# Kernel tuning notes

Measured on AMD Instinct MI355X. Metric: run time of the kernel, lower is better.

The kernel has to match this reference:

```python
import jax, jax.numpy as jnp
import numpy as np

N_NODES = 100_000
N_HYPEREDGES = 200_000
NNZ = 2_000_000
D = 64
H = 32
KEEP_RATIO = 0.5


def setup_inputs() -> dict:
    key = jax.random.key(0)
    ks = jax.random.split(key, 5)
    x = jax.random.normal(ks[0], (N_NODES, D), jnp.float32)
    V_idx = jax.random.randint(ks[1], (NNZ,), 0, N_NODES)
    E_idx = jax.random.randint(ks[2], (NNZ,), 0, N_HYPEREDGES)
    W1 = jax.random.normal(ks[3], (2 * D, H), jnp.float32) * (1.0 / np.sqrt(2 * D))
    b1 = jnp.zeros((H,), jnp.float32)
    W2 = jax.random.normal(ks[4], (H, 1), jnp.float32) * (1.0 / np.sqrt(H))
    b2 = jnp.zeros((1,), jnp.float32)
    return dict(x=x, V_idx=V_idx, E_idx=E_idx, W1=W1, b1=b1, W2=W2, b2=b2)


def _segment_mean(vals, idx, num_segments):
    # index_add sum / clamped count, matching reduce_incidence_to_edge / index_mean
    s = jax.ops.segment_sum(vals, idx, num_segments=num_segments)
    c = jax.ops.segment_sum(jnp.ones((vals.shape[0],), vals.dtype), idx,
                            num_segments=num_segments)
    c = jnp.clip(c, 1.0, None)
    if vals.ndim == 2:
        c = c[:, None]
    return s / c


def reference(x, V_idx, E_idx, W1, b1, W2, b2):
    xv = x[V_idx]                                   # [nnz, D] gather
    edge_feats = _segment_mean(xv, E_idx, N_HYPEREDGES)  # [E, D]
    pair = jnp.concatenate([xv, edge_feats[E_idx]], axis=-1)  # [nnz, 2D]
    h = jax.nn.relu(pair @ W1 + b1)                 # [nnz, H]
    probs = jax.nn.sigmoid((h @ W2 + b2)[:, 0])     # [nnz]

    k = max(1, int(KEEP_RATIO * NNZ))
    keep_ids = jax.lax.top_k(probs, k)[1]           # is_test=True path (deterministic)
    hard = jnp.zeros_like(probs).at[keep_ids].set(1.0)
    soft = jax.lax.stop_gradient(hard - probs) + probs  # straight-through

    edge_probs = _segment_mean(jax.lax.stop_gradient(probs), E_idx, N_HYPEREDGES)
    edge_soft = _segment_mean(soft, E_idx, N_HYPEREDGES)
    edge_hard = (_segment_mean(hard, E_idx, N_HYPEREDGES) > 0).astype(jnp.float32)
    return (probs, soft, hard, edge_probs, edge_soft, edge_hard)
```

## Files before the change

kernel.cpp:

```cpp
#include <hip/hip_runtime.h>
#include <math.h>

#define N_NODES   100000
#define N_EDGES   200000
#define NNZ       2000000
#define K_KEEP    1000000
#define BANDCAP   131072
#define TIECAP    4096
#define DELTA     1.0e-4f
#define SCAN_BLOCKS 196
#define USCALE (4294967296.0 / 4.0e-3)

#define SC_PASSES 8
#define SC_EPP    (N_EDGES / SC_PASSES)
#define SC_BLOCKS 2048

#define OFF_PAB   ((size_t)0)
#define OFF_PB32  ((size_t)25600000)
#define OFF_VJ    ((size_t)33600000)
#define OFF_RANK  ((size_t)49600000)
#define OFF_EOFF  ((size_t)57600000)
#define OFF_CUR   ((size_t)58400000)
#define OFF_BS    ((size_t)59200000)
#define OFF_BANDP ((size_t)59201024)
#define OFF_BANDJ ((size_t)59725312)
#define OFF_BANDE ((size_t)60249600)
#define OFF_BANDV ((size_t)60773888)
#define OFF_BANDK ((size_t)61298176)
#define OFF_TIEK  ((size_t)62346752)
#define OFF_TIEJ  ((size_t)62379520)
#define OFF_TIEP  ((size_t)62395904)
#define OFF_FLAG  ((size_t)62412288)
#define OFF_ECNT  ((size_t)64412288)
#define OFF_HIST  ((size_t)65212288)
#define OFF_ST    ((size_t)65245056)
#define ZERO_OFF  OFF_FLAG
#define ZERO_LEN  ((size_t)(65245312 - 62412288))

struct SelState {
    unsigned int B1;
    unsigned int rem1;
    float lo_edge, hi_edge;
    unsigned int bB1;
    unsigned int brem1;
    unsigned int bU0;
    unsigned int brem2;
    unsigned int _pad0[8];
    unsigned int n_hi;      unsigned int _pad1[15];
    unsigned int band_n;    unsigned int _pad2[15];
    unsigned int tie_n;     unsigned int _pad3[15];
};

__device__ __forceinline__ unsigned int band_u32(double key, float lo) {
    double t = (key - (double)lo) * USCALE;
    t = t < 0.0 ? 0.0 : (t > 4294967295.0 ? 4294967295.0 : t);
    return (unsigned int)t;
}

__global__ void proj_kernel(const float* __restrict__ x, const float* __restrict__ W1,
                            float2* __restrict__ p_ab2) {
    __shared__ float sW[128 * 32];
    __shared__ float sx[8][64];
    for (int t = threadIdx.x; t < 128 * 32; t += 256) sW[t] = W1[t];
    int base = blockIdx.x * 8;
    for (int t = threadIdx.x; t < 512; t += 256) {
        int n = t >> 6, d = t & 63;
        int g = base + n;
        sx[n][d] = (g < N_NODES) ? x[(size_t)g * 64 + d] : 0.f;
    }
    __syncthreads();
    int ln = threadIdx.x >> 5;
    int k  = threadIdx.x & 31;
    int node = base + ln;
    if (node >= N_NODES) return;
    float sa = 0.f, sb = 0.f;
    for (int d = 0; d < 64; ++d) {
        float xv = sx[ln][d];
        sa += xv * sW[d * 32 + k];
        sb += xv * sW[(64 + d) * 32 + k];
    }
    p_ab2[(size_t)node * 32 + k] = make_float2(sa, sb);
}

__global__ void count_rank_kernel(const int* __restrict__ E, unsigned int* __restrict__ edge_cnt,
                                  unsigned int* __restrict__ rank) {
    unsigned int base = blockIdx.x * 2048 + threadIdx.x;
    int ev[8];
    unsigned int rr[8];
    #pragma unroll
    for (int c = 0; c < 8; ++c) {
        unsigned int j = base + 256u * c;
        if (j < NNZ) ev[c] = E[j];
    }
    #pragma unroll
    for (int c = 0; c < 8; ++c) {
        unsigned int j = base + 256u * c;
        if (j < NNZ) rr[c] = atomicAdd(&edge_cnt[ev[c]], 1u);
    }
    #pragma unroll
    for (int c = 0; c < 8; ++c) {
        unsigned int j = base + 256u * c;
        if (j < NNZ) rank[j] = rr[c];
    }
}

__global__ void scanA_kernel(const unsigned int* __restrict__ edge_cnt,
                             unsigned int* __restrict__ edge_off, unsigned int* __restrict__ bsums) {
    __shared__ unsigned int s[256];
    int tid = threadIdx.x;
    int base = blockIdx.x * 1024 + tid * 4;
    unsigned int v0 = (base + 0 < N_EDGES) ? edge_cnt[base + 0] : 0u;
    unsigned int v1 = (base + 1 < N_EDGES) ? edge_cnt[base + 1] : 0u;
    unsigned int v2 = (base + 2 < N_EDGES) ? edge_cnt[base + 2] : 0u;
    unsigned int v3 = (base + 3 < N_EDGES) ? edge_cnt[base + 3] : 0u;
    unsigned int tsum = v0 + v1 + v2 + v3;
    s[tid] = tsum;
    __syncthreads();
    for (int off = 1; off < 256; off <<= 1) {
        unsigned int t = (tid >= off) ? s[tid - off] : 0u;
        __syncthreads();
        s[tid] += t;
        __syncthreads();
    }
    unsigned int excl = s[tid] - tsum;
    if (base + 0 < N_EDGES) edge_off[base + 0] = excl;
    if (base + 1 < N_EDGES) edge_off[base + 1] = excl + v0;
    if (base + 2 < N_EDGES) edge_off[base + 2] = excl + v0 + v1;
    if (base + 3 < N_EDGES) edge_off[base + 3] = excl + v0 + v1 + v2;
    if (tid == 255) bsums[blockIdx.x] = s[255];
}

__global__ void scanB_kernel(unsigned int* __restrict__ bsums) {
    __shared__ unsigned int s[256];
    int tid = threadIdx.x;
    unsigned int v = (tid < SCAN_BLOCKS) ? bsums[tid] : 0u;
    s[tid] = v;
    __syncthreads();
    for (int off = 1; off < 256; off <<= 1) {
        unsigned int t = (tid >= off) ? s[tid - off] : 0u;
        __syncthreads();
        s[tid] += t;
        __syncthreads();
    }
    if (tid < SCAN_BLOCKS) bsums[tid] = s[tid] - v;
}

__global__ void scanC_kernel(unsigned int* __restrict__ edge_off, const unsigned int* __restrict__ bsums) {
    int i = blockIdx.x * 256 + threadIdx.x;
    if (i >= N_EDGES) return;
    edge_off[i] = edge_off[i] + bsums[i >> 10];
}

__global__ void scatter_kernel(const int* __restrict__ V, const int* __restrict__ E,
                               const unsigned int* __restrict__ edge_off,
                               const unsigned int* __restrict__ rank,
                               uint2* __restrict__ vj) {
    unsigned int pass = blockIdx.x & 7u;
    unsigned int q    = blockIdx.x >> 3;
    unsigned int elo  = pass * SC_EPP;
    const unsigned int stride = (SC_BLOCKS / 8) * 256;
    for (unsigned int j = q * 256u + threadIdx.x; j < NNZ; j += stride) {
        unsigned int e = (unsigned int)__builtin_nontemporal_load(E + j);
        if (e - elo < (unsigned int)SC_EPP) {
            unsigned int pp = edge_off[e] + __builtin_nontemporal_load(rank + j);
            unsigned int v  = (unsigned int)__builtin_nontemporal_load(V + j);
            vj[pp] = make_uint2(v, j);
        }
    }
}

__global__ void edge_logit_kernel(const uint2* __restrict__ vj,
                                  const unsigned int* __restrict__ edge_off,
                                  const unsigned int* __restrict__ edge_cnt,
                                  const float2* __restrict__ p_ab2,
                                  const float* __restrict__ b1, const float* __restrict__ W2,
                                  const float* __restrict__ b2,
                                  float* __restrict__ probs_b, float* __restrict__ o_ep) {
    __shared__ float slog[4][32];
    __shared__ unsigned int sv[4][32];
    int e = blockIdx.x * 4 + (threadIdx.x >> 6);
    if (e >= N_EDGES) return;
    int w    = threadIdx.x >> 6;
    int lane = threadIdx.x & 63;
    int g    = lane >> 4;
    int l    = lane & 15;

    unsigned int off = edge_off[e];
    unsigned int deg = edge_cnt[e];
    unsigned int mind = deg < 32u ? deg : 32u;

    if ((unsigned int)lane < mind) sv[w][lane] = vj[off + lane].x;

    float2 w2  = ((const float2*)W2)[l];
    float2 bb1 = ((const float2*)b1)[l];
    float  b2v = b2[0];

    float2 aA[8];
    float2 bacc = make_float2(0.f, 0.f);
    #pragma unroll 8
    for (unsigned int m = 0; m < 8u; ++m) {
        if (4u * m >= mind) break;
        unsigned int idx = 4u * m + (unsigned int)g;
        if (idx < mind) {
            unsigned int v = sv[w][idx];
            float4 r = reinterpret_cast<const float4*>(p_ab2 + (size_t)v * 32u)[l];
            aA[m] = make_float2(r.x, r.z);
            bacc.x += r.y;
            bacc.y += r.w;
        } else {
            aA[m] = make_float2(0.f, 0.f);
        }
    }
    for (unsigned int ii = 32u + (unsigned int)g; ii < deg; ii += 4u) {
        unsigned int v = vj[off + ii].x;
        float4 r = reinterpret_cast<const float4*>(p_ab2 + (size_t)v * 32u)[l];
        bacc.x += r.y;
        bacc.y += r.w;
    }
    bacc.x += __shfl_xor(bacc.x, 16);
    bacc.y += __shfl_xor(bacc.y, 16);
    bacc.x += __shfl_xor(bacc.x, 32);
    bacc.y += __shfl_xor(bacc.y, 32);
    float cc = (float)(deg > 1u ? deg : 1u);
    float2 em2 = make_float2(bacc.x / cc + bb1.x, bacc.y / cc + bb1.y);

    #pragma unroll 8
    for (unsigned int m = 0; m < 8u; ++m) {
        if (4u * m >= mind) break;
        unsigned int idx = 4u * m + (unsigned int)g;
        float h0 = aA[m].x + em2.x;
        float h1 = aA[m].y + em2.y;
        h0 = h0 > 0.f ? h0 : 0.f;
        h1 = h1 > 0.f ? h1 : 0.f;
        float t = h0 * w2.x + h1 * w2.y;
        #pragma unroll
        for (int o = 8; o > 0; o >>= 1) t += __shfl_down(t, o, 16);
        if (l == 0 && idx < mind) slog[w][idx] = t;
    }
    float prsum = 0.f;
    if ((unsigned int)lane < mind) {
        float pr = 1.f / (1.f + __expf(-(slog[w][lane] + b2v)));
        probs_b[off + lane] = pr;
        prsum = pr;
    }
    for (unsigned int ii = 32u + (unsigned int)g; ii < deg; ii += 4u) {
        unsigned int v = vj[off + ii].x;
        float4 r = reinterpret_cast<const float4*>(p_ab2 + (size_t)v * 32u)[l];
        float h0 = r.x + em2.x;
        float h1 = r.z + em2.y;
        h0 = h0 > 0.f ? h0 : 0.f;
        h1 = h1 > 0.f ? h1 : 0.f;
        float t = h0 * w2.x + h1 * w2.y;
        #pragma unroll
        for (int o = 8; o > 0; o >>= 1) t += __shfl_down(t, o, 16);
        if (l == 0) {
            float pr = 1.f / (1.f + __expf(-(t + b2v)));
            probs_b[off + ii] = pr;
            prsum += pr;
        }
    }
    #pragma unroll
    for (int o = 32; o > 0; o >>= 1) prsum += __shfl_down(prsum, o, 64);
    if (lane == 0) o_ep[e] = prsum / cc;
}

__global__ void hist1_kernel(const float* __restrict__ probs_b, unsigned int* __restrict__ hist) {
    __shared__ unsigned int lh[2048];
    for (int t = threadIdx.x; t < 2048; t += 256) lh[t] = 0;
    __syncthreads();
    for (unsigned int i = blockIdx.x * 256 + threadIdx.x; i < NNZ; i += gridDim.x * 256) {
        unsigned int key = __float_as_uint(probs_b[i]);
        atomicAdd(&lh[key >> 21], 1u);
    }
    __syncthreads();
    for (int t = threadIdx.x; t < 2048; t += 256)
        if (lh[t]) atomicAdd(&hist[t], lh[t]);
}

__global__ void hist2_kernel(const float* __restrict__ probs_b, const SelState* __restrict__ st,
                             unsigned int* __restrict__ hist) {
    __shared__ unsigned int lh[2048];
    for (int t = threadIdx.x; t < 2048; t += 256) lh[t] = 0;
    __syncthreads();
    unsigned int B1 = st->B1;
    for (unsigned int i = blockIdx.x * 256 + threadIdx.x; i < NNZ; i += gridDim.x * 256) {
        unsigned int key = __float_as_uint(probs_b[i]);
        if ((key >> 21) == B1) atomicAdd(&lh[(key >> 10) & 2047u], 1u);
    }
    __syncthreads();
    for (int t = threadIdx.x; t < 2048; t += 256)
        if (lh[t]) atomicAdd(&hist[2048 + t], lh[t]);
}

__global__ void scan_sel_kernel(const unsigned int* __restrict__ hist, SelState* __restrict__ st, int which) {
    __shared__ unsigned int csum[256];
    int t = threadIdx.x;
    unsigned int target = (which == 0) ? (unsigned int)K_KEEP : st->rem1;
    const unsigned int* h = hist + (which ? 2048 : 0);
    unsigned int b[8];
    unsigned int s = 0;
    #pragma unroll
    for (int i = 0; i < 8; ++i) { b[i] = h[t * 8 + i]; s += b[i]; }
    csum[t] = s;
    __syncthreads();
    for (int off = 1; off < 256; off <<= 1) {
        unsigned int v = (t + off < 256) ? csum[t + off] : 0u;
        __syncthreads();
        csum[t] += v;
        __syncthreads();
    }
    unsigned int above = csum[t] - s;
    if (above < target && target <= above + s) {
        unsigned int rem = target - above;
        unsigned int cum = 0;
        #pragma unroll
        for (int i = 7; i >= 0; --i) {
            if (rem <= cum + b[i]) {
                unsigned int bin = (unsigned int)(t * 8 + i);
                if (which == 0) { st->B1 = bin; st->rem1 = rem - cum; }
                else {
                    unsigned int P = (st->B1 << 21) | (bin << 10);
                    st->lo_edge = __uint_as_float(P) - DELTA;
                    st->hi_edge = __uint_as_float(P + 1024u) + DELTA;
                }
                break;
            }
            cum += b[i];
        }
    }
}

__global__ void bandsel_kernel(const float* __restrict__ probs_b, const int* __restrict__ E,
                               const uint2* __restrict__ vj,
                               SelState* __restrict__ st,
                               unsigned int* __restrict__ band_p, unsigned int* __restrict__ band_j,
                               unsigned int* __restrict__ band_e, unsigned int* __restrict__ band_v) {
    __shared__ unsigned int whi[4], wband[4];
    __shared__ unsigned int sbase, scur;
    float hi = st->hi_edge, lo = st->lo_edge;
    unsigned int nhi = 0, nband = 0;
    for (unsigned int p = blockIdx.x * 256 + threadIdx.x; p < NNZ; p += gridDim.x * 256) {
        float pk = probs_b[p];
        if (pk > hi) nhi++;
        else if (pk >= lo) nband++;
    }
    #pragma unroll
    for (int o = 32; o > 0; o >>= 1) {
        nhi   += __shfl_down(nhi, o);
        nband += __shfl_down(nband, o);
    }
    if ((threadIdx.x & 63) == 0) { whi[threadIdx.x >> 6] = nhi; wband[threadIdx.x >> 6] = nband; }
    __syncthreads();
    if (threadIdx.x == 0) {
        unsigned int th = whi[0] + whi[1] + whi[2] + whi[3];
        unsigned int tb = wband[0] + wband[1] + wband[2] + wband[3];
        if (th) atomicAdd(&st->n_hi, th);
        sbase = tb ? atomicAdd(&st->band_n, tb) : 0u;
        scur = 0;
    }
    __syncthreads();
    for (unsigned int p = blockIdx.x * 256 + threadIdx.x; p < NNZ; p += gridDim.x * 256) {
        float pk = probs_b[p];
        if (pk <= hi && pk >= lo) {
            unsigned int s = sbase + atomicAdd(&scur, 1u);
            if (s < BANDCAP) {
                uint2 t = vj[p];
                band_p[s] = p;
                band_j[s] = t.y;
                band_e[s] = (unsigned int)E[t.y];
                band_v[s] = t.x;
            }
        }
    }
}

__global__ void rescue_kernel(const uint2* __restrict__ vj,
                              const unsigned int* __restrict__ edge_off,
                              const unsigned int* __restrict__ edge_cnt,
                              const float* __restrict__ x, const float* __restrict__ W1,
                              const float* __restrict__ b1, const float* __restrict__ W2,
                              const float* __restrict__ b2,
                              const unsigned int* __restrict__ band_e,
                              const unsigned int* __restrict__ band_v,
                              const SelState* __restrict__ st,
                              unsigned long long* __restrict__ band_key) {
    unsigned int n = st->band_n; if (n > BANDCAP) n = BANDCAP;
    if (blockIdx.x * 8 >= n) return;
    __shared__ float sW[128 * 32];
    for (int t = threadIdx.x; t < 128 * 32; t += 256) sW[t] = W1[t];
    __syncthreads();
    unsigned int g = blockIdx.x * 8 + (threadIdx.x >> 5);
    if (g >= n) return;
    int k = threadIdx.x & 31;
    unsigned int v = band_v[g];
    unsigned int e = band_e[g];
    unsigned int off = edge_off[e];
    unsigned int deg = edge_cnt[e];

    const float* xv = x + (size_t)v * 64u;
    double a = 0.0;
    #pragma unroll 8
    for (int d = 0; d < 64; ++d) a += (double)xv[d] * (double)sW[d * 32 + k];
    double bsum = 0.0;
    for (unsigned int m = off; m < off + deg; ++m) {
        const float* xm = x + (size_t)vj[m].x * 64u;
        double acc = 0.0;
        #pragma unroll 8
        for (int d = 0; d < 64; ++d) acc += (double)xm[d] * (double)sW[(64 + d) * 32 + k];
        bsum += acc;
    }
    double cc = (double)(deg > 1u ? deg : 1u);
    double h = a + bsum / cc + (double)b1[k];
    h = h > 0.0 ? h : 0.0;
    double t = h * (double)W2[k];
    #pragma unroll
    for (int o = 16; o > 0; o >>= 1) t += __shfl_down(t, o, 32);
    if (k == 0) {
        double pr = 1.0 / (1.0 + exp(-(t + (double)b2[0])));
        band_key[g] = (unsigned long long)__double_as_longlong(pr);
    }
}

__global__ void bhist1_kernel(const unsigned long long* __restrict__ band_key,
                              const SelState* __restrict__ st, unsigned int* __restrict__ hist) {
    __shared__ unsigned int lh[2048];
    for (int t = threadIdx.x; t < 2048; t += 256) lh[t] = 0;
    __syncthreads();
    unsigned int n = st->band_n; if (n > BANDCAP) n = BANDCAP;
    float lo = st->lo_edge;
    for (unsigned int i = blockIdx.x * 256 + threadIdx.x; i < n; i += gridDim.x * 256) {
        unsigned int u = band_u32(__longlong_as_double((long long)band_key[i]), lo);
        atomicAdd(&lh[u >> 21], 1u);
    }
    __syncthreads();
    for (int t = threadIdx.x; t < 2048; t += 256)
        if (lh[t]) atomicAdd(&hist[4096 + t], lh[t]);
}

__global__ void bhist2_kernel(const unsigned long long* __restrict__ band_key,
                              const SelState* __restrict__ st, unsigned int* __restrict__ hist) {
    __shared__ unsigned int lh[2048];
    for (int t = threadIdx.x; t < 2048; t += 256) lh[t] = 0;
    __syncthreads();
    unsigned int n = st->band_n; if (n > BANDCAP) n = BANDCAP;
    float lo = st->lo_edge;
    unsigned int bB1 = st->bB1;
    for (unsigned int i = blockIdx.x * 256 + threadIdx.x; i < n; i += gridDim.x * 256) {
        unsigned int u = band_u32(__longlong_as_double((long long)band_key[i]), lo);
        if ((u >> 21) == bB1) atomicAdd(&lh[(u >> 10) & 2047u], 1u);
    }
    __syncthreads();
    for (int t = threadIdx.x; t < 2048; t += 256)
        if (lh[t]) atomicAdd(&hist[6144 + t], lh[t]);
}

__global__ void bscan_kernel(const unsigned int* __restrict__ hist, SelState* __restrict__ st, int which) {
    __shared__ unsigned int csum[256];
    int t = threadIdx.x;
    unsigned int target = (which == 0) ? ((unsigned int)K_KEEP - st->n_hi) : st->brem1;
    const unsigned int* h = hist + (which ? 6144 : 4096);
    unsigned int b[8];
    unsigned int s = 0;
    #pragma unroll
    for (int i = 0; i < 8; ++i) { b[i] = h[t * 8 + i]; s += b[i]; }
    csum[t] = s;
    __syncthreads();
    for (int off = 1; off < 256; off <<= 1) {
        unsigned int v = (t + off < 256) ? csum[t + off] : 0u;
        __syncthreads();
        csum[t] += v;
        __syncthreads();
    }
    unsigned int above = csum[t] - s;
    if (above < target && target <= above + s) {
        unsigned int rem = target - above;
        unsigned int cum = 0;
        #pragma unroll
        for (int i = 7; i >= 0; --i) {
            if (rem <= cum + b[i]) {
                unsigned int bin = (unsigned int)(t * 8 + i);
                if (which == 0) { st->bB1 = bin; st->brem1 = rem - cum; }
                else            { st->bU0 = (st->bB1 << 21) | (bin << 10); st->brem2 = rem - cum; }
                break;
            }
            cum += b[i];
        }
    }
}

__global__ void btie_kernel(const unsigned long long* __restrict__ band_key,
                            const unsigned int* __restrict__ band_j,
                            const unsigned int* __restrict__ band_p,
                            SelState* __restrict__ st, unsigned char* __restrict__ flag,
                            unsigned long long* __restrict__ tie_k,
                            unsigned int* __restrict__ tie_j, unsigned int* __restrict__ tie_p) {
    unsigned int n = st->band_n; if (n > BANDCAP) n = BANDCAP;
    unsigned int i = blockIdx.x * 256 + threadIdx.x;
    if (i >= n) return;
    float lo = st->lo_edge;
    unsigned int U0 = st->bU0;
    unsigned long long key = band_key[i];
    unsigned int u = band_u32(__longlong_as_double((long long)key), lo);
    if (u >= U0 + 1024u) {
        flag[band_p[i]] = 2u;
    } else if (u >= U0) {
        unsigned int s = atomicAdd(&st->tie_n, 1u);
        if (s < TIECAP) { tie_k[s] = key; tie_j[s] = band_j[i]; tie_p[s] = band_p[i]; }
    }
}

__global__ void btierank_kernel(const unsigned long long* __restrict__ tie_k,
                                const unsigned int* __restrict__ tie_j,
                                const unsigned int* __restrict__ tie_p,
                                const SelState* __restrict__ st, unsigned char* __restrict__ flag) {
    unsigned int n = st->tie_n; if (n > TIECAP) n = TIECAP;
    unsigned int need = st->brem2;
    for (unsigned int i = threadIdx.x; i < n; i += 256) {
        unsigned long long ki = tie_k[i];
        unsigned int ji = tie_j[i];
        unsigned int r = 0;
        for (unsigned int q = 0; q < n; ++q) {
            unsigned long long kq = tie_k[q];
            if (kq > ki || (kq == ki && tie_j[q] < ji)) r++;
        }
        if (r < need) flag[tie_p[i]] = 2u;
    }
}

__global__ void out_kernel(const float* __restrict__ probs_b, const unsigned char* __restrict__ flag,
                           const int* __restrict__ E, const unsigned int* __restrict__ rank,
                           const unsigned int* __restrict__ edge_off, const SelState* __restrict__ st,
                           float* __restrict__ o_probs, float* __restrict__ o_soft, float* __restrict__ o_hard) {
    unsigned int j = blockIdx.x * 256 + threadIdx.x;
    if (j >= NNZ) return;
    float hi = st->hi_edge;
    unsigned int p = edge_off[E[j]] + rank[j];
    float pk = probs_b[p];
    float hb = (pk > hi || flag[p] == 2u) ? 1.f : 0.f;
    o_probs[j] = pk;
    o_soft[j]  = hb;
    o_hard[j]  = hb;
}

__global__ void edge_out_kernel(const float* __restrict__ probs_b, const unsigned char* __restrict__ flag,
                                const unsigned int* __restrict__ edge_off,
                                const unsigned int* __restrict__ edge_cnt,
                                const SelState* __restrict__ st,
                                float* __restrict__ o_es, float* __restrict__ o_eh) {
    unsigned int e = blockIdx.x * 256 + threadIdx.x;
    if (e >= N_EDGES) return;
    float hi = st->hi_edge;
    unsigned int off = edge_off[e], deg = edge_cnt[e];
    unsigned int cnt = 0;
    for (unsigned int i = 0; i < deg; ++i)
        cnt += (probs_b[off + i] > hi || flag[off + i] == 2u) ? 1u : 0u;
    float cc = (float)(deg > 1u ? deg : 1u);
    o_es[e] = (float)cnt / cc;
    o_eh[e] = cnt ? 1.f : 0.f;
}

extern "C" void kernel_launch(void* const* d_in, const int* in_sizes, int n_in,
                              void* d_out, int out_size, void* d_ws, size_t ws_size,
                              hipStream_t stream) {
    const float* x  = (const float*)d_in[0];
    const int*   V  = (const int*)d_in[1];
    const int*   E  = (const int*)d_in[2];
    const float* W1 = (const float*)d_in[3];
    const float* b1 = (const float*)d_in[4];
    const float* W2 = (const float*)d_in[5];
    const float* b2 = (const float*)d_in[6];

    float* out     = (float*)d_out;
    float* o_probs = out;
    float* o_soft  = out + NNZ;
    float* o_hard  = out + 2 * (size_t)NNZ;
    float* o_ep    = out + 3 * (size_t)NNZ;
    float* o_es    = out + 3 * (size_t)NNZ + N_EDGES;
    float* o_eh    = out + 3 * (size_t)NNZ + 2 * (size_t)N_EDGES;

    char* w = (char*)d_ws;
    float2*             p_ab2    = (float2*)(w + OFF_PAB);
    float*              probs_b  = (float*)(w + OFF_PB32);
    uint2*              vj       = (uint2*)(w + OFF_VJ);
    unsigned int*       rank     = (unsigned int*)(w + OFF_RANK);
    unsigned int*       edge_off = (unsigned int*)(w + OFF_EOFF);
    unsigned int*       bsums    = (unsigned int*)(w + OFF_BS);
    unsigned int*       band_p   = (unsigned int*)(w + OFF_BANDP);
    unsigned int*       band_j   = (unsigned int*)(w + OFF_BANDJ);
    unsigned int*       band_e   = (unsigned int*)(w + OFF_BANDE);
    unsigned int*       band_v   = (unsigned int*)(w + OFF_BANDV);
    unsigned long long* band_key = (unsigned long long*)(w + OFF_BANDK);
    unsigned long long* tie_k    = (unsigned long long*)(w + OFF_TIEK);
    unsigned int*       tie_j    = (unsigned int*)(w + OFF_TIEJ);
    unsigned int*       tie_p    = (unsigned int*)(w + OFF_TIEP);
    unsigned char*      flag     = (unsigned char*)(w + OFF_FLAG);
    unsigned int*       edge_cnt = (unsigned int*)(w + OFF_ECNT);
    unsigned int*       hist     = (unsigned int*)(w + OFF_HIST);
    SelState*           st       = (SelState*)(w + OFF_ST);

    hipMemsetAsync(w + ZERO_OFF, 0, ZERO_LEN, stream);

    proj_kernel<<<(N_NODES + 7) / 8, 256, 0, stream>>>(x, W1, p_ab2);

    count_rank_kernel<<<(NNZ + 2047) / 2048, 256, 0, stream>>>(E, edge_cnt, rank);
    scanA_kernel<<<SCAN_BLOCKS, 256, 0, stream>>>(edge_cnt, edge_off, bsums);
    scanB_kernel<<<1, 256, 0, stream>>>(bsums);
    scanC_kernel<<<(N_EDGES + 255) / 256, 256, 0, stream>>>(edge_off, bsums);
    scatter_kernel<<<SC_BLOCKS, 256, 0, stream>>>(V, E, edge_off, rank, vj);

    edge_logit_kernel<<<(N_EDGES + 3) / 4, 256, 0, stream>>>(vj, edge_off, edge_cnt,
                                                             p_ab2, b1, W2, b2, probs_b, o_ep);

    hist1_kernel<<<1024, 256, 0, stream>>>(probs_b, hist);
    scan_sel_kernel<<<1, 256, 0, stream>>>(hist, st, 0);
    hist2_kernel<<<1024, 256, 0, stream>>>(probs_b, st, hist);
    scan_sel_kernel<<<1, 256, 0, stream>>>(hist, st, 1);

    bandsel_kernel<<<1024, 256, 0, stream>>>(probs_b, E, vj, st,
                                             band_p, band_j, band_e, band_v);
    rescue_kernel<<<BANDCAP / 8, 256, 0, stream>>>(vj, edge_off, edge_cnt, x, W1, b1, W2, b2,
                                                   band_e, band_v, st, band_key);

    bhist1_kernel<<<64, 256, 0, stream>>>(band_key, st, hist);
    bscan_kernel<<<1, 256, 0, stream>>>(hist, st, 0);
    bhist2_kernel<<<64, 256, 0, stream>>>(band_key, st, hist);
    bscan_kernel<<<1, 256, 0, stream>>>(hist, st, 1);
    btie_kernel<<<BANDCAP / 256, 256, 0, stream>>>(band_key, band_j, band_p, st, flag,
                                                   tie_k, tie_j, tie_p);
    btierank_kernel<<<1, 256, 0, stream>>>(tie_k, tie_j, tie_p, st, flag);

    out_kernel<<<(NNZ + 255) / 256, 256, 0, stream>>>(probs_b, flag, E, rank, edge_off, st,
                                                      o_probs, o_soft, o_hard);
    edge_out_kernel<<<(N_EDGES + 255) / 256, 256, 0, stream>>>(probs_b, flag, edge_off, edge_cnt, st,
                                                               o_es, o_eh);
}
```

Measured before the change: 562.6 us.

## Fold radix-select scans into consumer kernels and vectorize histogram and output passes

Removes the four single-block scan kernels by having every block of the following kernel redo the 2048-bin prefix scan in shared memory. This cuts launch count and serialization gaps. The first histogram now reads float4 and spreads atomics over four sub-histograms to reduce shared-memory contention. The output kernel handles four elements per thread with vector loads and stores. The cost is redundant scan work in every block and extra barriers at the start of the consumer kernels. Also, btie_kernel writes bU0/brem2 from every block, which btierank reads later.

Measured after the change: 556.7 us. Within noise of the previous version (-1.0%).

```diff
diff --git a/kernel.cpp b/kernel.cpp
--- a/kernel.cpp
+++ b/kernel.cpp
@@ -264,39 +264,11 @@
     if (lane == 0) o_ep[e] = prsum / cc;
 }
 
-__global__ void hist1_kernel(const float* __restrict__ probs_b, unsigned int* __restrict__ hist) {
-    __shared__ unsigned int lh[2048];
-    for (int t = threadIdx.x; t < 2048; t += 256) lh[t] = 0;
-    __syncthreads();
-    for (unsigned int i = blockIdx.x * 256 + threadIdx.x; i < NNZ; i += gridDim.x * 256) {
-        unsigned int key = __float_as_uint(probs_b[i]);
-        atomicAdd(&lh[key >> 21], 1u);
-    }
-    __syncthreads();
-    for (int t = threadIdx.x; t < 2048; t += 256)
-        if (lh[t]) atomicAdd(&hist[t], lh[t]);
-}
-
-__global__ void hist2_kernel(const float* __restrict__ probs_b, const SelState* __restrict__ st,
-                             unsigned int* __restrict__ hist) {
-    __shared__ unsigned int lh[2048];
-    for (int t = threadIdx.x; t < 2048; t += 256) lh[t] = 0;
-    __syncthreads();
-    unsigned int B1 = st->B1;
-    for (unsigned int i = blockIdx.x * 256 + threadIdx.x; i < NNZ; i += gridDim.x * 256) {
-        unsigned int key = __float_as_uint(probs_b[i]);
-        if ((key >> 21) == B1) atomicAdd(&lh[(key >> 10) & 2047u], 1u);
-    }
-    __syncthreads();
-    for (int t = threadIdx.x; t < 2048; t += 256)
-        if (lh[t]) atomicAdd(&hist[2048 + t], lh[t]);
-}
-
-__global__ void scan_sel_kernel(const unsigned int* __restrict__ hist, SelState* __restrict__ st, int which) {
-    __shared__ unsigned int csum[256];
+__device__ __forceinline__ void radix_sel_256(const unsigned int* __restrict__ h,
+                                              unsigned int target,
+                                              unsigned int* csum, unsigned int* sres,
+                                              unsigned int& out_bin, unsigned int& out_rem) {
     int t = threadIdx.x;
-    unsigned int target = (which == 0) ? (unsigned int)K_KEEP : st->rem1;
-    const unsigned int* h = hist + (which ? 2048 : 0);
     unsigned int b[8];
     unsigned int s = 0;
     #pragma unroll
@@ -316,28 +288,75 @@
         #pragma unroll
         for (int i = 7; i >= 0; --i) {
             if (rem <= cum + b[i]) {
-                unsigned int bin = (unsigned int)(t * 8 + i);
-                if (which == 0) { st->B1 = bin; st->rem1 = rem - cum; }
-                else {
-                    unsigned int P = (st->B1 << 21) | (bin << 10);
-                    st->lo_edge = __uint_as_float(P) - DELTA;
-                    st->hi_edge = __uint_as_float(P + 1024u) + DELTA;
-                }
+                sres[0] = (unsigned int)(t * 8 + i);
+                sres[1] = rem - cum;
                 break;
             }
             cum += b[i];
         }
     }
+    __syncthreads();
+    out_bin = sres[0];
+    out_rem = sres[1];
+    __syncthreads();
+}
+
+__global__ void hist1_kernel(const float* __restrict__ probs_b, unsigned int* __restrict__ hist) {
+    __shared__ unsigned int lh[4][2048 + 8];
+    for (int t = threadIdx.x; t < 4 * (2048 + 8); t += 256) ((unsigned int*)lh)[t] = 0;
+    __syncthreads();
+    int sub = threadIdx.x & 3;
+    const float4* p4 = (const float4*)probs_b;
+    for (unsigned int i = blockIdx.x * 256 + threadIdx.x; i < NNZ / 4; i += gridDim.x * 256) {
+        float4 v = p4[i];
+        atomicAdd(&lh[sub][__float_as_uint(v.x) >> 21], 1u);
+        atomicAdd(&lh[sub][__float_as_uint(v.y) >> 21], 1u);
+        atomicAdd(&lh[sub][__float_as_uint(v.z) >> 21], 1u);
+        atomicAdd(&lh[sub][__float_as_uint(v.w) >> 21], 1u);
+    }
+    __syncthreads();
+    for (int t = threadIdx.x; t < 2048; t += 256) {
+        unsigned int s = lh[0][t] + lh[1][t] + lh[2][t] + lh[3][t];
+        if (s) atomicAdd(&hist[t], s);
+    }
+}
+
+__global__ void hist2_kernel(const float* __restrict__ probs_b,
+                             const unsigned int* __restrict__ hist_ro,
+                             unsigned int* __restrict__ hist) {
+    __shared__ unsigned int csum[256];
+    __shared__ unsigned int sres[2];
+    __shared__ unsigned int lh[2048];
+    unsigned int B1, rem_unused;
+    radix_sel_256(hist_ro, (unsigned int)K_KEEP, csum, sres, B1, rem_unused);
+    for (int t = threadIdx.x; t < 2048; t += 256) lh[t] = 0;
+    __syncthreads();
+    for (unsigned int i = blockIdx.x * 256 + threadIdx.x; i < NNZ; i += gridDim.x * 256) {
+        unsigned int key = __float_as_uint(probs_b[i]);
+        if ((key >> 21) == B1) atomicAdd(&lh[(key >> 10) & 2047u], 1u);
+    }
+    __syncthreads();
+    for (int t = threadIdx.x; t < 2048; t += 256)
+        if (lh[t]) atomicAdd(&hist[2048 + t], lh[t]);
 }
 
 __global__ void bandsel_kernel(const float* __restrict__ probs_b, const int* __restrict__ E,
                                const uint2* __restrict__ vj,
+                               const unsigned int* __restrict__ hist,
                                SelState* __restrict__ st,
                                unsigned int* __restrict__ band_p, unsigned int* __restrict__ band_j,
                                unsigned int* __restrict__ band_e, unsigned int* __restrict__ band_v) {
+    __shared__ unsigned int csum[256];
+    __shared__ unsigned int sres[2];
     __shared__ unsigned int whi[4], wband[4];
     __shared__ unsigned int sbase, scur;
-    float hi = st->hi_edge, lo = st->lo_edge;
+    unsigned int B1, rem1, bin2, rem2_unused;
+    radix_sel_256(hist, (unsigned int)K_KEEP, csum, sres, B1, rem1);
+    radix_sel_256(hist + 2048, rem1, csum, sres, bin2, rem2_unused);
+    unsigned int P = (B1 << 21) | (bin2 << 10);
+    float lo = __uint_as_float(P) - DELTA;
+    float hi = __uint_as_float(P + 1024u) + DELTA;
+    if (threadIdx.x == 0) { st->lo_edge = lo; st->hi_edge = hi; }
     unsigned int nhi = 0, nband = 0;
     for (unsigned int p = blockIdx.x * 256 + threadIdx.x; p < NNZ; p += gridDim.x * 256) {
         float pk = probs_b[p];
@@ -439,12 +458,15 @@
 
 __global__ void bhist2_kernel(const unsigned long long* __restrict__ band_key,
                               const SelState* __restrict__ st, unsigned int* __restrict__ hist) {
+    __shared__ unsigned int csum[256];
+    __shared__ unsigned int sres[2];
     __shared__ unsigned int lh[2048];
+    unsigned int bB1, rem_unused;
+    radix_sel_256(hist + 4096, (unsigned int)K_KEEP - st->n_hi, csum, sres, bB1, rem_unused);
     for (int t = threadIdx.x; t < 2048; t += 256) lh[t] = 0;
     __syncthreads();
     unsigned int n = st->band_n; if (n > BANDCAP) n = BANDCAP;
     float lo = st->lo_edge;
-    unsigned int bB1 = st->bB1;
     for (unsigned int i = blockIdx.x * 256 + threadIdx.x; i < n; i += gridDim.x * 256) {
         unsigned int u = band_u32(__longlong_as_double((long long)band_key[i]), lo);
         if ((u >> 21) == bB1) atomicAdd(&lh[(u >> 10) & 2047u], 1u);
@@ -454,51 +476,24 @@
         if (lh[t]) atomicAdd(&hist[6144 + t], lh[t]);
 }
 
-__global__ void bscan_kernel(const unsigned int* __restrict__ hist, SelState* __restrict__ st, int which) {
-    __shared__ unsigned int csum[256];
-    int t = threadIdx.x;
-    unsigned int target = (which == 0) ? ((unsigned int)K_KEEP - st->n_hi) : st->brem1;
-    const unsigned int* h = hist + (which ? 6144 : 4096);
-    unsigned int b[8];
-    unsigned int s = 0;
-    #pragma unroll
-    for (int i = 0; i < 8; ++i) { b[i] = h[t * 8 + i]; s += b[i]; }
-    csum[t] = s;
-    __syncthreads();
-    for (int off = 1; off < 256; off <<= 1) {
-        unsigned int v = (t + off < 256) ? csum[t + off] : 0u;
-        __syncthreads();
-        csum[t] += v;
-        __syncthreads();
-    }
-    unsigned int above = csum[t] - s;
-    if (above < target && target <= above + s) {
-        unsigned int rem = target - above;
-        unsigned int cum = 0;
-        #pragma unroll
-        for (int i = 7; i >= 0; --i) {
-            if (rem <= cum + b[i]) {
-                unsigned int bin = (unsigned int)(t * 8 + i);
-                if (which == 0) { st->bB1 = bin; st->brem1 = rem - cum; }
-                else            { st->bU0 = (st->bB1 << 21) | (bin << 10); st->brem2 = rem - cum; }
-                break;
-            }
-            cum += b[i];
-        }
-    }
-}
-
 __global__ void btie_kernel(const unsigned long long* __restrict__ band_key,
                             const unsigned int* __restrict__ band_j,
                             const unsigned int* __restrict__ band_p,
+                            const unsigned int* __restrict__ hist,
                             SelState* __restrict__ st, unsigned char* __restrict__ flag,
                             unsigned long long* __restrict__ tie_k,
                             unsigned int* __restrict__ tie_j, unsigned int* __restrict__ tie_p) {
+    __shared__ unsigned int csum[256];
+    __shared__ unsigned int sres[2];
+    unsigned int bB1, brem1, bin2, brem2;
+    radix_sel_256(hist + 4096, (unsigned int)K_KEEP - st->n_hi, csum, sres, bB1, brem1);
+    radix_sel_256(hist + 6144, brem1, csum, sres, bin2, brem2);
+    unsigned int U0 = (bB1 << 21) | (bin2 << 10);
+    if (threadIdx.x == 0) { st->bU0 = U0; st->brem2 = brem2; }
     unsigned int n = st->band_n; if (n > BANDCAP) n = BANDCAP;
     unsigned int i = blockIdx.x * 256 + threadIdx.x;
     if (i >= n) return;
     float lo = st->lo_edge;
-    unsigned int U0 = st->bU0;
     unsigned long long key = band_key[i];
     unsigned int u = band_u32(__longlong_as_double((long long)key), lo);
     if (u >= U0 + 1024u) {
@@ -531,15 +526,25 @@
                            const int* __restrict__ E, const unsigned int* __restrict__ rank,
                            const unsigned int* __restrict__ edge_off, const SelState* __restrict__ st,
                            float* __restrict__ o_probs, float* __restrict__ o_soft, float* __restrict__ o_hard) {
-    unsigned int j = blockIdx.x * 256 + threadIdx.x;
-    if (j >= NNZ) return;
+    unsigned int j0 = (blockIdx.x * 256 + threadIdx.x) * 4u;
+    if (j0 >= NNZ) return;
     float hi = st->hi_edge;
-    unsigned int p = edge_off[E[j]] + rank[j];
-    float pk = probs_b[p];
-    float hb = (pk > hi || flag[p] == 2u) ? 1.f : 0.f;
-    o_probs[j] = pk;
-    o_soft[j]  = hb;
-    o_hard[j]  = hb;
+    int4  e4 = *reinterpret_cast<const int4*>(E + j0);
+    uint4 r4 = *reinterpret_cast<const uint4*>(rank + j0);
+    unsigned int p0 = edge_off[e4.x] + r4.x;
+    unsigned int p1 = edge_off[e4.y] + r4.y;
+    unsigned int p2 = edge_off[e4.z] + r4.z;
+    unsigned int p3 = edge_off[e4.w] + r4.w;
+    float pk0 = probs_b[p0], pk1 = probs_b[p1], pk2 = probs_b[p2], pk3 = probs_b[p3];
+    unsigned char f0 = flag[p0], f1 = flag[p1], f2 = flag[p2], f3 = flag[p3];
+    float4 pr = make_float4(pk0, pk1, pk2, pk3);
+    float4 hb = make_float4((pk0 > hi || f0 == 2u) ? 1.f : 0.f,
+                            (pk1 > hi || f1 == 2u) ? 1.f : 0.f,
+                            (pk2 > hi || f2 == 2u) ? 1.f : 0.f,
+                            (pk3 > hi || f3 == 2u) ? 1.f : 0.f);
+    *reinterpret_cast<float4*>(o_probs + j0) = pr;
+    *reinterpret_cast<float4*>(o_soft  + j0) = hb;
+    *reinterpret_cast<float4*>(o_hard  + j0) = hb;
 }
 
 __global__ void edge_out_kernel(const float* __restrict__ probs_b, const unsigned char* __restrict__ flag,
@@ -612,25 +617,20 @@
                                                              p_ab2, b1, W2, b2, probs_b, o_ep);
 
     hist1_kernel<<<1024, 256, 0, stream>>>(probs_b, hist);
-    scan_sel_kernel<<<1, 256, 0, stream>>>(hist, st, 0);
-    hist2_kernel<<<1024, 256, 0, stream>>>(probs_b, st, hist);
-    scan_sel_kernel<<<1, 256, 0, stream>>>(hist, st, 1);
-
-    bandsel_kernel<<<1024, 256, 0, stream>>>(probs_b, E, vj, st,
+    hist2_kernel<<<1024, 256, 0, stream>>>(probs_b, hist, hist);
+    bandsel_kernel<<<1024, 256, 0, stream>>>(probs_b, E, vj, hist, st,
                                              band_p, band_j, band_e, band_v);
     rescue_kernel<<<BANDCAP / 8, 256, 0, stream>>>(vj, edge_off, edge_cnt, x, W1, b1, W2, b2,
                                                    band_e, band_v, st, band_key);
 
     bhist1_kernel<<<64, 256, 0, stream>>>(band_key, st, hist);
-    bscan_kernel<<<1, 256, 0, stream>>>(hist, st, 0);
     bhist2_kernel<<<64, 256, 0, stream>>>(band_key, st, hist);
-    bscan_kernel<<<1, 256, 0, stream>>>(hist, st, 1);
-    btie_kernel<<<BANDCAP / 256, 256, 0, stream>>>(band_key, band_j, band_p, st, flag,
+    btie_kernel<<<BANDCAP / 256, 256, 0, stream>>>(band_key, band_j, band_p, hist, st, flag,
                                                    tie_k, tie_j, tie_p);
     btierank_kernel<<<1, 256, 0, stream>>>(tie_k, tie_j, tie_p, st, flag);
 
-    out_kernel<<<(NNZ + 255) / 256, 256, 0, stream>>>(probs_b, flag, E, rank, edge_off, st,
-                                                      o_probs, o_soft, o_hard);
+    out_kernel<<<(NNZ / 4 + 255) / 256, 256, 0, stream>>>(probs_b, flag, E, rank, edge_off, st,
+                                                          o_probs, o_soft, o_hard);
     edge_out_kernel<<<(N_EDGES + 255) / 256, 256, 0, stream>>>(probs_b, flag, edge_off, edge_cnt, st,
                                                                o_es, o_eh);
 }
```
